# Optimization experiments

Measured on AMD Instinct MI355X. Metric: run time of the kernel, lower is better.

## Reference

```python
import jax, jax.numpy as jnp
import numpy as np

N_STATES = 8
LBW = 128          # look_back_window == seq_len L (required by the einsum)
PRED_W = 16        # prediction_window
C = 16             # look_back_channel_dim
B = 512
LOG2PI = float(np.log(2.0 * np.pi))


def setup_inputs() -> dict:
    key = jax.random.key(0)
    k0, k1, k2, k3, k4 = jax.random.split(key, 5)
    emissions = jax.random.normal(k0, (B, LBW, C), jnp.float32)
    transition_matrix = jax.random.normal(k1, (N_STATES, N_STATES), jnp.float32)
    initial_distribution = jax.random.normal(k2, (N_STATES,), jnp.float32)
    means = jax.random.normal(k3, (N_STATES, C), jnp.float32)
    covar_chol = jnp.tile(jnp.eye(C, dtype=jnp.float32)[None], (N_STATES, 1, 1))
    W = jax.random.normal(k4, (N_STATES, LBW, C, C), jnp.float32) * 0.01
    return {"emissions": emissions, "transition_matrix": transition_matrix,
            "initial_distribution": initial_distribution, "means": means,
            "covar_chol": covar_chol, "W": W}


def reference(emissions, transition_matrix, initial_distribution, means, covar_chol, W):
    Bs, L, Cc = emissions.shape
    S = means.shape[0]
    lbw = W.shape[1]

    # --- positive-definite covariances from Cholesky factors (exp on diagonal) ---
    d = jnp.diagonal(covar_chol, axis1=-2, axis2=-1)                 # (S, C)
    chol = jnp.tril(covar_chol, -1) + jax.vmap(jnp.diag)(jnp.exp(d)) # (S, C, C)
    covar = chol @ jnp.swapaxes(chol, -1, -2) + 1e-6 * jnp.eye(Cc, dtype=emissions.dtype)
    prec = jnp.linalg.inv(covar)                                     # (S, C, C)
    Lc = jnp.linalg.cholesky(covar)
    logdet = 2.0 * jnp.sum(jnp.log(jnp.diagonal(Lc, axis1=-2, axis2=-1)), axis=-1)  # (S,)

    # --- per-step Gaussian log-likelihood with linear AR mean ---
    # causal zero-padded history: window f, element l = padded[f + l]
    padded = jnp.concatenate([jnp.zeros_like(emissions), emissions], axis=1)  # (B, 2L, C)
    idx = jnp.arange(L)[:, None] + jnp.arange(L)[None, :]                     # (L, L)
    inputs = padded[:, idx, :]                                                # (B, L, L, C)
    ar = jnp.einsum('bflc,slcd->bsfd', inputs, W)                             # (B, S, L, C)
    diff = emissions[:, None] - (ar + means[None, :, None])                   # (B, S, L, C)
    quad = jnp.einsum('bslc,scd,bsld->bsl', diff, prec, diff)                 # (B, S, L)
    emis_ll = -0.5 * (quad + logdet[None, :, None] + Cc * LOG2PI)
    emis_ll = jnp.transpose(emis_ll, (0, 2, 1))                               # (B, L, S)

    # --- HMM forward algorithm (log-space scan over time) ---
    log_trans = jnp.log(jax.nn.softmax(transition_matrix, axis=1) + 1e-8)     # (S, S)
    la0 = jnp.log(jax.nn.softmax(initial_distribution)) + emis_ll[:, 0]       # (B, S)

    def step(la, e_t):
        la = jax.nn.logsumexp(la[:, :, None] + log_trans[None], axis=1) + e_t
        return la, None

    la_last, _ = jax.lax.scan(step, la0, jnp.transpose(emis_ll[:, 1:], (1, 0, 2)))

    trans = jax.nn.softmax(transition_matrix, axis=1)
    state = jnp.argmax(la_last, axis=1)                                       # (B,)
    buf = emissions[:, -lbw:]                                                 # (B, lbw, C)
    preds = []
    for _ in range(PRED_W):
        state = jnp.argmax(trans[state], axis=1)
        pred = jnp.einsum('blc,blcd->bd', buf, W[state]) + means[state]       # (B, C)
        preds.append(pred)
        buf = jnp.concatenate([buf[:, 1:], pred[:, None]], axis=1)
    return jnp.stack(preds, axis=1)                                           # (B, PRED_W, C)
```

## Files before the change

### kernel.cpp

```cpp
#include <hip/hip_runtime.h>
#include <hip/hip_bf16.h>

#define LOG2PI_F 1.8378770664093453f
#define LOG2E_F  1.44269504f

typedef float f32x4 __attribute__((ext_vector_type(4)));
typedef short s16x8 __attribute__((ext_vector_type(8)));
typedef unsigned short u16;

#define OFF_PREC   0
#define OFF_LOGDET 2048
#define OFF_LTR    2064
#define OFF_LINI   2128
#define OFF_CHAIN  2144
#define OFF_CNT    2272
#define OFF_PERM   2304
#define OFF_ELL    8192
#define OFF_WT     532480

__device__ inline u16 f2bf(float x) {
  union { float f; unsigned u; } v; v.f = x;
  unsigned r = v.u + 0x7fffu + ((v.u >> 16) & 1u);
  return (u16)(r >> 16);
}

__device__ inline float fexp2(float x) {
#if __has_builtin(__builtin_amdgcn_exp2f)
  return __builtin_amdgcn_exp2f(x);
#else
  return exp2f(x);
#endif
}
__device__ inline float flog2(float x) {
#if __has_builtin(__builtin_amdgcn_logf)
  return __builtin_amdgcn_logf(x);
#else
  return log2f(x);
#endif
}

__global__ __launch_bounds__(256) void prep_wt_kernel(const float* __restrict__ tmat,
                                                      const float* __restrict__ initd,
                                                      const float* __restrict__ cc,
                                                      const float* __restrict__ W,
                                                      float* __restrict__ ws) {
  __shared__ float Ls[8][16][16];
  __shared__ float tmp[256];
  int t = threadIdx.x;

  if (blockIdx.x < 1024) {
    u16* Wt = (u16*)(ws + OFF_WT);
    int sl = blockIdx.x;
    tmp[t] = W[sl * 256 + t];
    __syncthreads();
    int d = t >> 4, c = t & 15;
    Wt[sl * 256 + t] = f2bf(tmp[c * 16 + d]);
    return;
  }

  float* prec   = ws + OFF_PREC;
  float* logdet = ws + OFF_LOGDET;
  float* ltr    = ws + OFF_LTR;
  float* lini   = ws + OFF_LINI;
  int*   chain  = (int*)(ws + OFF_CHAIN);

  if (t < 128) {
    int s = t >> 4, i = t & 15;
    const float* c0 = cc + s * 256 + i * 16;
    for (int j = 0; j < 16; ++j) {
      float v = c0[j];
      Ls[s][i][j] = (i > j) ? v : (i == j ? expf(v) : 0.f);
    }
  } else if (t < 136) {
    int s = t - 128;
    float ld = 0.f;
    for (int i = 0; i < 16; ++i) ld += cc[s * 256 + i * 17];
    logdet[s] = 2.f * ld;
  } else if (t == 136) {
    float m = -1e30f;
    for (int i = 0; i < 8; ++i) m = fmaxf(m, initd[i]);
    float sum = 0.f;
    for (int i = 0; i < 8; ++i) sum += expf(initd[i] - m);
    float lsum = logf(sum);
    for (int i = 0; i < 8; ++i) lini[i] = (initd[i] - m - lsum) * LOG2E_F;
  } else if (t == 137) {
    int nxt[8];
    for (int i = 0; i < 8; ++i) {
      float best = -1e30f; int bi = 0;
      for (int j = 0; j < 8; ++j) {
        float v = tmat[i * 8 + j];
        if (v > best) { best = v; bi = j; }
      }
      nxt[i] = bi;
    }
    for (int s0 = 0; s0 < 8; ++s0) {
      int c = s0;
      for (int k = 0; k < 16; ++k) { c = nxt[c]; chain[s0 * 16 + k] = c; }
    }
  } else if (t == 138) {
    int* cnt = (int*)(ws + OFF_CNT);
    for (int i = 0; i < 8; ++i) cnt[i] = 0;
  } else if (t >= 144 && t < 152) {
    int i = t - 144;
    float m = -1e30f;
    for (int j = 0; j < 8; ++j) m = fmaxf(m, tmat[i * 8 + j]);
    float sum = 0.f;
    for (int j = 0; j < 8; ++j) sum += expf(tmat[i * 8 + j] - m);
    for (int j = 0; j < 8; ++j)
      ltr[i * 8 + j] = logf(expf(tmat[i * 8 + j] - m) / sum + 1e-8f) * LOG2E_F;
  }
  __syncthreads();
  if (t < 128) {
    int s = t >> 4, col = t & 15;
    float y[16], x[16];
#pragma unroll
    for (int i = 0; i < 16; ++i) {
      float v = (i == col) ? 1.f : 0.f;
#pragma unroll
      for (int k = 0; k < 16; ++k) if (k < i) v -= Ls[s][i][k] * y[k];
      y[i] = v / Ls[s][i][i];
    }
#pragma unroll
    for (int i = 15; i >= 0; --i) {
      float v = y[i];
#pragma unroll
      for (int k = 0; k < 16; ++k) if (k > i) v -= Ls[s][k][i] * x[k];
      x[i] = v / Ls[s][i][i];
    }
#pragma unroll
    for (int i = 0; i < 16; ++i) prec[s * 256 + i * 16 + col] = x[i];
  }
}

__global__ __launch_bounds__(512, 4) void emis_kernel(const float* __restrict__ emis,
                                                      const float* __restrict__ means,
                                                      float* __restrict__ ws) {
  const float* prec   = ws + OFF_PREC;
  const float* logdet = ws + OFF_LOGDET;
  const u16* Wt = (const u16*)(ws + OFF_WT);
  float* ell = ws + OFF_ELL;

  int sp = blockIdx.x & 3;
  int bg = blockIdx.x >> 2;
  int s0 = sp * 2;
  int bb0 = bg * 4;
  int tid = threadIdx.x;

  __shared__ __align__(16) char smem[40960];
  char* pbase = smem;
  float* dlf = (float*)smem;
  const s16x8 zero8 = {0, 0, 0, 0, 0, 0, 0, 0};

  for (int i = tid; i < 1024; i += 512)
    *(s16x8*)(pbase + (i >> 8) * 8192 + (i & 255) * 16) = zero8;
  for (int i = tid; i < 1024; i += 512) {
    int g = i >> 8, erow = (i >> 1) & 127, h2 = i & 1;
    const f32x4* src = (const f32x4*)(emis + (size_t)(bb0 + g) * 2048 + erow * 16 + h2 * 8);
    f32x4 v0 = src[0], v1 = src[1];
    s16x8 pk;
#pragma unroll
    for (int c = 0; c < 4; ++c) { pk[c] = (short)f2bf(v0[c]); pk[c + 4] = (short)f2bf(v1[c]); }
    int row = 128 + erow;
    int off = ((row << 5) + (h2 << 4)) ^ (((row >> 2) & 3) << 4);
    *(s16x8*)(pbase + g * 8192 + off) = pk;
  }
  __syncthreads();

  int wave = tid >> 6, lane = tid & 63;
  int mt = (wave < 4) ? wave : 11 - wave;
  int rc = lane & 15;
  int h  = (lane >> 4) & 1;
  int dl = lane >> 5;
  int hh = h << 4;
  int kst = 56 - 8 * mt;
  int r0 = mt * 16 + rc + dl;

  const u16* Bp0 = Wt + ((size_t)((s0 * 128 + dl) * 16 + rc) * 16) + h * 8 + (size_t)kst * 512;
  const u16* Bp1 = Bp0 + 32768;

  f32x4 acc[2][4] = {};
  s16x8 w0 = *(const s16x8*)Bp0, w1 = *(const s16x8*)Bp1;
  for (int kk = kst; kk < 64; ++kk) {
    s16x8 n0, n1;
    if (kk < 63) { n0 = *(const s16x8*)(Bp0 + 512); n1 = *(const s16x8*)(Bp1 + 512); }
    Bp0 += 512; Bp1 += 512;
    int row = r0 + 2 * kk;
    const char* pa = pbase + (((row << 5) + hh) ^ (((row >> 2) & 3) << 4));
#pragma unroll
    for (int g = 0; g < 4; ++g) {
      s16x8 a = *(const s16x8*)(pa + g * 8192);
      acc[0][g] = __builtin_amdgcn_mfma_f32_16x16x32_bf16(a, w0, acc[0][g], 0, 0, 0);
      acc[1][g] = __builtin_amdgcn_mfma_f32_16x16x32_bf16(a, w1, acc[1][g], 0, 0, 0);
    }
    w0 = n0; w1 = n1;
  }

  int hi = (lane >> 4) & 3;
  float ev[4][4];
#pragma unroll
  for (int g = 0; g < 4; ++g)
#pragma unroll
    for (int r = 0; r < 4; ++r)
      ev[g][r] = emis[(size_t)(bb0 + g) * 2048 + (mt * 16 + hi * 4 + r) * 16 + rc];

  __syncthreads();

#pragma unroll
  for (int s = 0; s < 2; ++s) {
    float mn = means[(s0 + s) * 16 + rc];
#pragma unroll
    for (int g = 0; g < 4; ++g) {
#pragma unroll
      for (int r = 0; r < 4; ++r) {
        int f = mt * 16 + hi * 4 + r;
        dlf[(g * 128 + f) * 20 + rc] = ev[g][r] - acc[s][g][r] - mn;
      }
    }
    __syncthreads();
    const float* P = prec + (s0 + s) * 256;
    float c2 = -0.72134752f * (logdet[s0 + s] + 16.f * LOG2PI_F);
    {
      int g = tid >> 7, f = tid & 127;
      float dv[16];
#pragma unroll
      for (int c = 0; c < 4; ++c)
        *(f32x4*)&dv[c * 4] = *(const f32x4*)&dlf[(g * 128 + f) * 20 + c * 4];
      float qq = 0.f;
#pragma unroll
      for (int c = 0; c < 16; ++c) {
        float tsum = 0.5f * P[c * 16 + c] * dv[c];
#pragma unroll
        for (int d2 = 0; d2 < 16; ++d2)
          if (d2 > c) tsum = fmaf(P[c * 16 + d2], dv[d2], tsum);
        qq = fmaf(dv[c], tsum, qq);
      }
      ell[((size_t)(bb0 + g) * 8 + s0 + s) * 128 + f] = fmaf(-2.f * 0.72134752f, qq, c2);
    }
    if (s == 0) __syncthreads();
  }
}

__global__ __launch_bounds__(256) void fwd_kernel(float* __restrict__ ws) {
  const float* ell  = ws + OFF_ELL;
  const float* ltr  = ws + OFF_LTR;
  const float* lini = ws + OFF_LINI;
  int* cnt  = (int*)(ws + OFF_CNT);
  int* perm = (int*)(ws + OFF_PERM);

  __shared__ float leaf[128 * 68];
  __shared__ float lvl[64 * 68];
  __shared__ float ebuf[1024];
  __shared__ float LTs[64];
  __shared__ float redv[8];

  int b = blockIdx.x, tid = threadIdx.x;

  *(f32x4*)&ebuf[tid * 4] = *(const f32x4*)(ell + (size_t)b * 1024 + tid * 4);
  if (tid < 64) LTs[tid] = ltr[tid];
  __syncthreads();

  for (int t = tid; t < 8192; t += 256) {
    int m = t >> 6, i = (t >> 3) & 7, j = t & 7;
    float v;
    if (m < 127) v = LTs[i * 8 + j] + ebuf[j * 128 + (m + 1)];
    else         v = (i == j) ? 0.f : -1e30f;
    leaf[m * 68 + i * 8 + j] = v;
  }
  __syncthreads();

  float* src = leaf;
  float* dst = lvl;
  int nm = 64;
  for (int level = 0; level < 7; ++level) {
    for (int t = tid; t < nm * 8; t += 256) {
      int p = t >> 3, i = t & 7;
      const float* Ma = src + (p * 2) * 68 + i * 8;
      const float* Mb = src + (p * 2 + 1) * 68;
      float av[8];
      *(f32x4*)&av[0] = *(const f32x4*)&Ma[0];
      *(f32x4*)&av[4] = *(const f32x4*)&Ma[4];
      float B[8][8];
#pragma unroll
      for (int k = 0; k < 8; ++k) {
        *(f32x4*)&B[k][0] = *(const f32x4*)&Mb[k * 8];
        *(f32x4*)&B[k][4] = *(const f32x4*)&Mb[k * 8 + 4];
      }
      float outv[8];
#pragma unroll
      for (int j = 0; j < 8; ++j) {
        float sv[8];
#pragma unroll
        for (int k = 0; k < 8; ++k) sv[k] = av[k] + B[k][j];
        float m01 = fmaxf(sv[0], sv[1]), m23 = fmaxf(sv[2], sv[3]);
        float m45 = fmaxf(sv[4], sv[5]), m67 = fmaxf(sv[6], sv[7]);
        float m = fmaxf(fmaxf(m01, m23), fmaxf(m45, m67));
        float sum = ((fexp2(sv[0] - m) + fexp2(sv[1] - m))
                   + (fexp2(sv[2] - m) + fexp2(sv[3] - m)))
                  + ((fexp2(sv[4] - m) + fexp2(sv[5] - m))
                   + (fexp2(sv[6] - m) + fexp2(sv[7] - m)));
        outv[j] = m + flog2(sum);
      }
      *(f32x4*)&dst[p * 68 + i * 8]     = *(f32x4*)&outv[0];
      *(f32x4*)&dst[p * 68 + i * 8 + 4] = *(f32x4*)&outv[4];
    }
    __syncthreads();
    float* tswap = src; src = dst; dst = tswap;
    nm >>= 1;
  }

  if (tid < 8) {
    int s = tid;
    float sv[8];
#pragma unroll
    for (int i = 0; i < 8; ++i)
      sv[i] = lini[i] + ebuf[i * 128] + src[i * 8 + s];
    float m01 = fmaxf(sv[0], sv[1]), m23 = fmaxf(sv[2], sv[3]);
    float m45 = fmaxf(sv[4], sv[5]), m67 = fmaxf(sv[6], sv[7]);
    float m = fmaxf(fmaxf(m01, m23), fmaxf(m45, m67));
    float sum = ((fexp2(sv[0] - m) + fexp2(sv[1] - m))
               + (fexp2(sv[2] - m) + fexp2(sv[3] - m)))
              + ((fexp2(sv[4] - m) + fexp2(sv[5] - m))
               + (fexp2(sv[6] - m) + fexp2(sv[7] - m)));
    redv[s] = m + flog2(sum);
  }
  __syncthreads();
  if (tid == 0) {
    float best = -1e30f; int bi = 0;
#pragma unroll
    for (int i = 0; i < 8; ++i) {
      float o = redv[i];
      if (o > best) { best = o; bi = i; }
    }
    int pos = atomicAdd(&cnt[bi], 1);
    perm[bi * 512 + pos] = b;
  }
}

__global__ __launch_bounds__(512, 2) void pred_kernel(const float* __restrict__ emis,
                                                      const float* __restrict__ means,
                                                      float* __restrict__ ws,
                                                      float* __restrict__ out) {
  const int* chain = (const int*)(ws + OFF_CHAIN);
  const int* cnt   = (const int*)(ws + OFF_CNT);
  const int* perm  = (const int*)(ws + OFF_PERM);
  const u16* Wt = (const u16*)(ws + OFF_WT);

  __shared__ u16 buf[16][128][16];
  __shared__ float part[8][64][4];
  __shared__ float ms[8][16];
  __shared__ int bid[16];

  int bucket = blockIdx.x >> 5, slot = blockIdx.x & 31;
  int nb = cnt[bucket];
  int base = slot * 16;
  if (base >= nb) return;
  int tid = threadIdx.x;
  char* pb = (char*)&buf[0][0][0];

  if (tid < 16) {
    int idx = base + tid;
    bid[tid] = perm[bucket * 512 + (idx < nb ? idx : base)];
  } else if (tid >= 128 && tid < 256) {
    int t2 = tid - 128;
    ms[t2 >> 4][t2 & 15] = means[t2];
  }
  __syncthreads();

  for (int i = tid; i < 2048; i += 512) {
    int b = i >> 7, row = i & 127;
    const f32x4* sp = (const f32x4*)(emis + (size_t)bid[b] * 2048 + row * 16);
    f32x4 v0 = sp[0], v1 = sp[1], v2 = sp[2], v3 = sp[3];
    s16x8 p0, p1;
#pragma unroll
    for (int j = 0; j < 4; ++j) {
      p0[j] = (short)f2bf(v0[j]); p0[4 + j] = (short)f2bf(v1[j]);
      p1[j] = (short)f2bf(v2[j]); p1[4 + j] = (short)f2bf(v3[j]);
    }
    int xo = (b & 7) << 4;
    int bse = b * 4096 + row * 32;
    *(s16x8*)(pb + (bse ^ xo)) = p0;
    *(s16x8*)(pb + ((bse + 16) ^ xo)) = p1;
  }
  __syncthreads();

  int wave = tid >> 6, lane = tid & 63;
  int rc = lane & 15;
  int q  = lane >> 4;
  int h  = q & 1;
  int dl = q >> 1;
  int axor = (rc & 7) << 4;
  const int* mychain = chain + bucket * 16;
  int b_own = q * 4 + (wave & 3);
  int bown_base = b_own * 4096;
  int bown_xor = (b_own & 7) << 4;

  float outv[16];
  int start = 0;
#pragma unroll
  for (int k = 0; k < 16; ++k) {
    int st = mychain[k];
    const u16* Bb = Wt + ((size_t)((st * 128 + dl) * 16 + rc) * 16) + h * 8;
    f32x4 accA = {0.f, 0.f, 0.f, 0.f}, accB = {0.f, 0.f, 0.f, 0.f};
#pragma unroll
    for (int t2 = 0; t2 < 4; ++t2) {
      int kkA = wave * 8 + t2 * 2, kkB = kkA + 1;
      s16x8 wA = *(const s16x8*)(Bb + (size_t)kkA * 512);
      s16x8 wB2 = *(const s16x8*)(Bb + (size_t)kkB * 512);
      int rowA = (start + kkA * 2 + dl) & 127;
      int rowB = (start + kkB * 2 + dl) & 127;
      s16x8 aA = *(const s16x8*)(pb + ((rc * 4096 + rowA * 32 + h * 16) ^ axor));
      s16x8 aB = *(const s16x8*)(pb + ((rc * 4096 + rowB * 32 + h * 16) ^ axor));
      accA = __builtin_amdgcn_mfma_f32_16x16x32_bf16(aA, wA, accA, 0, 0, 0);
      accB = __builtin_amdgcn_mfma_f32_16x16x32_bf16(aB, wB2, accB, 0, 0, 0);
    }
    f32x4 acc = accA + accB;
    *(f32x4*)&part[wave][lane][0] = acc;
    __syncthreads();
    if (wave < 4) {
      f32x4 cs = (*(f32x4*)&part[0][lane][0] + *(f32x4*)&part[1][lane][0])
               + (*(f32x4*)&part[2][lane][0] + *(f32x4*)&part[3][lane][0]);
      f32x4 cs2 = (*(f32x4*)&part[4][lane][0] + *(f32x4*)&part[5][lane][0])
                + (*(f32x4*)&part[6][lane][0] + *(f32x4*)&part[7][lane][0]);
      cs = cs + cs2;
      float vown = (wave & 3) == 0 ? cs[0] : (wave & 3) == 1 ? cs[1]
                 : (wave & 3) == 2 ? cs[2] : cs[3];
      float o = vown + ms[st][rc];
      outv[k] = o;
      *(u16*)(pb + ((bown_base + start * 32 + rc * 2) ^ bown_xor)) = f2bf(o);
    }
    __syncthreads();
    start = (start + 1) & 127;
  }
  if (wave < 4 && base + b_own < nb) {
    float* op = out + (size_t)bid[b_own] * 256 + rc;
#pragma unroll
    for (int k = 0; k < 16; ++k) op[k * 16] = outv[k];
  }
}

extern "C" void kernel_launch(void* const* d_in, const int* in_sizes, int n_in,
                              void* d_out, int out_size, void* d_ws, size_t ws_size,
                              hipStream_t stream) {
  const float* emis  = (const float*)d_in[0];
  const float* tmat  = (const float*)d_in[1];
  const float* initd = (const float*)d_in[2];
  const float* means = (const float*)d_in[3];
  const float* cc    = (const float*)d_in[4];
  const float* W     = (const float*)d_in[5];
  float* ws  = (float*)d_ws;
  float* out = (float*)d_out;

  hipLaunchKernelGGL(prep_wt_kernel, dim3(1025), dim3(256), 0, stream, tmat, initd, cc, W, ws);
  hipLaunchKernelGGL(emis_kernel, dim3(512), dim3(512), 0, stream, emis, means, ws);
  hipLaunchKernelGGL(fwd_kernel, dim3(512), dim3(256), 0, stream, ws);
  hipLaunchKernelGGL(pred_kernel, dim3(256), dim3(512), 0, stream, emis, means, ws, out);
}
```

Before: 76.54 us.

## Replace log-space semiring tree reduction with scaled linear-space matrix products

The forward-algorithm tree reduction now works in linear probability space rather than log-space. Leaf matrices are exponentiated once against a per-step max, and each combine becomes a plain 8x8 FMA matrix product. Rows are then rescaled by a power of two taken from the row max exponent, shared across 8 lanes with shuffles. This removes most exp2/log2 evaluations in the reduction, at the risk of underflow or precision loss, since only a relative per-row scale is kept and the final argmax relies on the entries staying comparable.

```diff
diff --git a/kernel.cpp b/kernel.cpp
--- a/kernel.cpp
+++ b/kernel.cpp
@@ -29,13 +29,6 @@
   return __builtin_amdgcn_exp2f(x);
 #else
   return exp2f(x);
-#endif
-}
-__device__ inline float flog2(float x) {
-#if __has_builtin(__builtin_amdgcn_logf)
-  return __builtin_amdgcn_logf(x);
-#else
-  return log2f(x);
 #endif
 }
 
@@ -251,19 +244,32 @@
   __shared__ float lvl[64 * 68];
   __shared__ float ebuf[1024];
   __shared__ float LTs[64];
+  __shared__ float kmax[128];
   __shared__ float redv[8];
 
   int b = blockIdx.x, tid = threadIdx.x;
 
   *(f32x4*)&ebuf[tid * 4] = *(const f32x4*)(ell + (size_t)b * 1024 + tid * 4);
   if (tid < 64) LTs[tid] = ltr[tid];
+  __syncthreads();
+
+  if (tid < 128) {
+    int m = tid;
+    float mx = 0.f;
+    if (m < 127) {
+      mx = -1e30f;
+#pragma unroll
+      for (int j = 0; j < 8; ++j) mx = fmaxf(mx, ebuf[j * 128 + m + 1]);
+    }
+    kmax[m] = mx;
+  }
   __syncthreads();
 
   for (int t = tid; t < 8192; t += 256) {
     int m = t >> 6, i = (t >> 3) & 7, j = t & 7;
     float v;
-    if (m < 127) v = LTs[i * 8 + j] + ebuf[j * 128 + (m + 1)];
-    else         v = (i == j) ? 0.f : -1e30f;
+    if (m < 127) v = fexp2(LTs[i * 8 + j] + ebuf[j * 128 + (m + 1)] - kmax[m]);
+    else         v = (i == j) ? 1.f : 0.f;
     leaf[m * 68 + i * 8 + j] = v;
   }
   __syncthreads();
@@ -288,18 +294,20 @@
       float outv[8];
 #pragma unroll
       for (int j = 0; j < 8; ++j) {
-        float sv[8];
-#pragma unroll
-        for (int k = 0; k < 8; ++k) sv[k] = av[k] + B[k][j];
-        float m01 = fmaxf(sv[0], sv[1]), m23 = fmaxf(sv[2], sv[3]);
-        float m45 = fmaxf(sv[4], sv[5]), m67 = fmaxf(sv[6], sv[7]);
-        float m = fmaxf(fmaxf(m01, m23), fmaxf(m45, m67));
-        float sum = ((fexp2(sv[0] - m) + fexp2(sv[1] - m))
-                   + (fexp2(sv[2] - m) + fexp2(sv[3] - m)))
-                  + ((fexp2(sv[4] - m) + fexp2(sv[5] - m))
-                   + (fexp2(sv[6] - m) + fexp2(sv[7] - m)));
-        outv[j] = m + flog2(sum);
+        float sum = 0.f;
+#pragma unroll
+        for (int k = 0; k < 8; ++k) sum = fmaf(av[k], B[k][j], sum);
+        outv[j] = sum;
       }
+      float rm = outv[0];
+#pragma unroll
+      for (int j = 1; j < 8; ++j) rm = fmaxf(rm, outv[j]);
+      rm = fmaxf(rm, __shfl_xor(rm, 1));
+      rm = fmaxf(rm, __shfl_xor(rm, 2));
+      rm = fmaxf(rm, __shfl_xor(rm, 4));
+      int ex = (int)((__float_as_uint(rm) >> 23) & 0xFFu) - 127;
+#pragma unroll
+      for (int j = 0; j < 8; ++j) outv[j] = ldexpf(outv[j], -ex);
       *(f32x4*)&dst[p * 68 + i * 8]     = *(f32x4*)&outv[0];
       *(f32x4*)&dst[p * 68 + i * 8 + 4] = *(f32x4*)&outv[4];
     }
@@ -310,18 +318,14 @@
 
   if (tid < 8) {
     int s = tid;
-    float sv[8];
+    float k0 = -1e30f;
+#pragma unroll
+    for (int i = 0; i < 8; ++i) k0 = fmaxf(k0, lini[i] + ebuf[i * 128]);
+    float v = 0.f;
 #pragma unroll
     for (int i = 0; i < 8; ++i)
-      sv[i] = lini[i] + ebuf[i * 128] + src[i * 8 + s];
-    float m01 = fmaxf(sv[0], sv[1]), m23 = fmaxf(sv[2], sv[3]);
-    float m45 = fmaxf(sv[4], sv[5]), m67 = fmaxf(sv[6], sv[7]);
-    float m = fmaxf(fmaxf(m01, m23), fmaxf(m45, m67));
-    float sum = ((fexp2(sv[0] - m) + fexp2(sv[1] - m))
-               + (fexp2(sv[2] - m) + fexp2(sv[3] - m)))
-              + ((fexp2(sv[4] - m) + fexp2(sv[5] - m))
-               + (fexp2(sv[6] - m) + fexp2(sv[7] - m)));
-    redv[s] = m + flog2(sum);
+      v = fmaf(fexp2(lini[i] + ebuf[i * 128] - k0), src[i * 8 + s], v);
+    redv[s] = v;
   }
   __syncthreads();
   if (tid == 0) {
```

New measurement: 73.29 us. -4.2%, faster.
